# Kernel optimization log

Measured on AMD Instinct MI355X. Metric: run time of the kernel, lower is better.

Reference implementation:

```python
import jax, jax.numpy as jnp
import numpy as np

NUM_HEADS = 16
HEAD_DIM = 128
BLOCK_SIZE = 16
BATCH = 16
BLOCKS_PER_SEQ = 128            # max_context_len // BLOCK_SIZE
MAX_CONTEXT_LEN = BLOCKS_PER_SEQ * BLOCK_SIZE  # 2048
NUM_BLOCKS = 2048               # total physical KV blocks
NEG_BIG = -1e30


def setup_inputs() -> dict:
    key = jax.random.key(0)
    k1, k2, k3, k4, k5 = jax.random.split(key, 5)
    query = jax.random.normal(k1, (BATCH, NUM_HEADS, HEAD_DIM), dtype=jnp.float32)
    key_cache = jax.random.normal(k2, (NUM_BLOCKS, BLOCK_SIZE, NUM_HEADS, HEAD_DIM), dtype=jnp.float32)
    value_cache = jax.random.normal(k3, (NUM_BLOCKS, BLOCK_SIZE, NUM_HEADS, HEAD_DIM), dtype=jnp.float32)
    block_tables = jax.random.randint(k4, (BATCH, BLOCKS_PER_SEQ), 0, NUM_BLOCKS, dtype=jnp.int32)
    context_lens = jax.random.randint(k5, (BATCH,), 1, MAX_CONTEXT_LEN + 1, dtype=jnp.int32)
    return {
        "query": query,
        "key_cache": key_cache,
        "value_cache": value_cache,
        "block_tables": block_tables,
        "context_lens": context_lens,
        "max_context_len": MAX_CONTEXT_LEN,
    }


def reference(query, key_cache, value_cache, block_tables, context_lens, max_context_len):
    # Decode-path paged attention: query [B, H, D], cache [NB, BS, H, D].
    B, H, D = query.shape
    scale = jnp.asarray(D, query.dtype) ** -0.5
    # Gather logical KV via block-table indirection -> [B, nb, bs, H, D] -> [B, T, H, D]
    K = key_cache[block_tables].reshape(B, -1, H, D)[:, :max_context_len]
    V = value_cache[block_tables].reshape(B, -1, H, D)[:, :max_context_len]
    T = K.shape[1]
    scores = jnp.einsum("bhd,bthd->bht", query, K) * scale  # [B, H, T]
    valid = jnp.arange(T, dtype=jnp.int32)[None, :] < context_lens[:, None]  # [B, T]
    scores = jnp.where(valid[:, None, :], scores, NEG_BIG)
    probs = jax.nn.softmax(scores, axis=-1)
    out = jnp.einsum("bht,bthd->bhd", probs, V)  # [B, H, D]
    return out
```

## Files before the change

### kernel.cpp

```cpp
#include <hip/hip_runtime.h>

#define NUM_HEADS 16
#define HEAD_DIM 128
#define KV_BLOCK 16
#define BATCH 16
#define BLOCKS_PER_SEQ 128
#define MAX_CTX 2048
#define PART_TOKENS 256
#define NUM_PARTS (MAX_CTX / PART_TOKENS)
#define WS_STRIDE (HEAD_DIM + 2)
#define NEG_BIG -1e30f

__global__ __launch_bounds__(256) void paged_attn_partial(
    const float* __restrict__ q,
    const float* __restrict__ kcache,
    const float* __restrict__ vcache,
    const int*   __restrict__ block_tables,
    const int*   __restrict__ ctx_lens,
    float* __restrict__ ws)
{
    const int part = blockIdx.x;
    const int h    = blockIdx.y;
    const int b    = blockIdx.z;
    const int tid  = threadIdx.x;

    float* wsp = ws + ((size_t)((b * NUM_HEADS + h) * NUM_PARTS + part)) * WS_STRIDE;

    const int ctx = ctx_lens[b];
    const int t0  = part * PART_TOKENS;
    int valid_n = ctx - t0;
    if (valid_n > PART_TOKENS) valid_n = PART_TOKENS;

    if (valid_n <= 0) {
        if (tid < HEAD_DIM) wsp[tid] = 0.0f;
        if (tid == 0) { wsp[HEAD_DIM] = NEG_BIG; wsp[HEAD_DIM + 1] = 0.0f; }
        return;
    }

    __shared__ __align__(16) float sQ[HEAD_DIM];
    __shared__ float sScores[PART_TOKENS];
    __shared__ int   sBlocks[PART_TOKENS / KV_BLOCK];
    __shared__ __align__(16) float sAcc[8][HEAD_DIM];
    __shared__ float sRedMax[4], sRedSum[4];

    if (tid < HEAD_DIM) sQ[tid] = q[((size_t)b * NUM_HEADS + h) * HEAD_DIM + tid];
    if (tid < PART_TOKENS / KV_BLOCK)
        sBlocks[tid] = block_tables[b * BLOCKS_PER_SEQ + part * (PART_TOKENS / KV_BLOCK) + tid];
    __syncthreads();

    const int hw     = tid >> 5;
    const int lane32 = tid & 31;
    const float scale = 0.088388347648318447f;

    const float4 q4 = *(const float4*)(&sQ[lane32 * 4]);
    for (int t = hw; t < PART_TOKENS; t += 8) {
        float s;
        if (t < valid_n) {
            const int phys = sBlocks[t >> 4];
            const float* kptr = kcache +
                ((((size_t)phys * KV_BLOCK + (t & 15)) * NUM_HEADS + h) * HEAD_DIM);
            const float4 k4 = *(const float4*)(kptr + lane32 * 4);
            float d = k4.x * q4.x + k4.y * q4.y + k4.z * q4.z + k4.w * q4.w;
            #pragma unroll
            for (int off = 1; off < 32; off <<= 1)
                d += __shfl_xor(d, off, 64);
            s = d * scale;
        } else {
            s = NEG_BIG;
        }
        if (lane32 == 0) sScores[t] = s;
    }
    __syncthreads();

    float v = sScores[tid];
    float r = v;
    #pragma unroll
    for (int off = 32; off > 0; off >>= 1) r = fmaxf(r, __shfl_xor(r, off, 64));
    const int wid = tid >> 6;
    if ((tid & 63) == 0) sRedMax[wid] = r;
    __syncthreads();
    const float m = fmaxf(fmaxf(sRedMax[0], sRedMax[1]), fmaxf(sRedMax[2], sRedMax[3]));

    const float p = __expf(v - m);
    sScores[tid] = p;
    float s = p;
    #pragma unroll
    for (int off = 32; off > 0; off >>= 1) s += __shfl_xor(s, off, 64);
    if ((tid & 63) == 0) sRedSum[wid] = s;
    __syncthreads();
    const float l = sRedSum[0] + sRedSum[1] + sRedSum[2] + sRedSum[3];

    float4 acc = make_float4(0.f, 0.f, 0.f, 0.f);
    for (int t = hw; t < valid_n; t += 8) {
        const float pt = sScores[t];
        const int phys = sBlocks[t >> 4];
        const float* vptr = vcache +
            ((((size_t)phys * KV_BLOCK + (t & 15)) * NUM_HEADS + h) * HEAD_DIM);
        const float4 v4 = *(const float4*)(vptr + lane32 * 4);
        acc.x += pt * v4.x; acc.y += pt * v4.y; acc.z += pt * v4.z; acc.w += pt * v4.w;
    }
    *(float4*)(&sAcc[hw][lane32 * 4]) = acc;
    __syncthreads();

    if (tid < HEAD_DIM) {
        float o = 0.f;
        #pragma unroll
        for (int g = 0; g < 8; ++g) o += sAcc[g][tid];
        wsp[tid] = o;
    }
    if (tid == 0) { wsp[HEAD_DIM] = m; wsp[HEAD_DIM + 1] = l; }
}

__global__ __launch_bounds__(128) void paged_attn_reduce(
    const float* __restrict__ ws,
    float* __restrict__ out)
{
    const int bh  = blockIdx.x;
    const int tid = threadIdx.x;
    const float* base = ws + (size_t)bh * NUM_PARTS * WS_STRIDE;

    __shared__ float sM[NUM_PARTS], sL[NUM_PARTS];
    if (tid < NUM_PARTS) {
        sM[tid] = base[tid * WS_STRIDE + HEAD_DIM];
        sL[tid] = base[tid * WS_STRIDE + HEAD_DIM + 1];
    }
    __syncthreads();

    float M = NEG_BIG;
    #pragma unroll
    for (int p = 0; p < NUM_PARTS; ++p) M = fmaxf(M, sM[p]);

    float w[NUM_PARTS];
    float L = 0.f;
    #pragma unroll
    for (int p = 0; p < NUM_PARTS; ++p) {
        const float wi = (sL[p] > 0.f) ? __expf(sM[p] - M) : 0.f;
        w[p] = wi;
        L += wi * sL[p];
    }

    float o = 0.f;
    #pragma unroll
    for (int p = 0; p < NUM_PARTS; ++p)
        o += w[p] * base[p * WS_STRIDE + tid];

    out[(size_t)bh * HEAD_DIM + tid] = o / L;
}

extern "C" void kernel_launch(void* const* d_in, const int* in_sizes, int n_in,
                              void* d_out, int out_size, void* d_ws, size_t ws_size,
                              hipStream_t stream) {
    const float* q  = (const float*)d_in[0];
    const float* k  = (const float*)d_in[1];
    const float* v  = (const float*)d_in[2];
    const int*   bt = (const int*)d_in[3];
    const int*   cl = (const int*)d_in[4];
    float* out = (float*)d_out;
    float* ws  = (float*)d_ws;

    dim3 grid1(NUM_PARTS, NUM_HEADS, BATCH);
    paged_attn_partial<<<grid1, 256, 0, stream>>>(q, k, v, bt, cl, ws);

    dim3 grid2(BATCH * NUM_HEADS);
    paged_attn_reduce<<<grid2, 128, 0, stream>>>(ws, out);
}
```

Before: 451.5 us.

## Fuse QK and PV passes into single online-softmax loop with K/V prefetch

Replaces the three-phase scores/softmax/PV structure with a single pass where each half-warp keeps its own running max, sum and accumulator and merges them at the end. K and V for the next token are loaded one iteration ahead to overlap memory latency with compute, and the scale is folded into Q. This removes the shared score buffer and two block barriers. In exchange it adds per-token exponentials for rescaling and serial dependence on the running max.

```diff
diff --git a/kernel.cpp b/kernel.cpp
--- a/kernel.cpp
+++ b/kernel.cpp
@@ -10,6 +10,7 @@
 #define NUM_PARTS (MAX_CTX / PART_TOKENS)
 #define WS_STRIDE (HEAD_DIM + 2)
 #define NEG_BIG -1e30f
+#define TOKEN_STRIDE (NUM_HEADS * HEAD_DIM)
 
 __global__ __launch_bounds__(256) void paged_attn_partial(
     const float* __restrict__ q,
@@ -27,8 +28,7 @@
     float* wsp = ws + ((size_t)((b * NUM_HEADS + h) * NUM_PARTS + part)) * WS_STRIDE;
 
     const int ctx = ctx_lens[b];
-    const int t0  = part * PART_TOKENS;
-    int valid_n = ctx - t0;
+    int valid_n = ctx - part * PART_TOKENS;
     if (valid_n > PART_TOKENS) valid_n = PART_TOKENS;
 
     if (valid_n <= 0) {
@@ -38,77 +38,78 @@
     }
 
     __shared__ __align__(16) float sQ[HEAD_DIM];
-    __shared__ float sScores[PART_TOKENS];
     __shared__ int   sBlocks[PART_TOKENS / KV_BLOCK];
     __shared__ __align__(16) float sAcc[8][HEAD_DIM];
-    __shared__ float sRedMax[4], sRedSum[4];
+    __shared__ float sM[8], sL[8];
 
-    if (tid < HEAD_DIM) sQ[tid] = q[((size_t)b * NUM_HEADS + h) * HEAD_DIM + tid];
+    if (tid < HEAD_DIM)
+        sQ[tid] = q[((size_t)b * NUM_HEADS + h) * HEAD_DIM + tid] * 0.088388347648318447f;
     if (tid < PART_TOKENS / KV_BLOCK)
         sBlocks[tid] = block_tables[b * BLOCKS_PER_SEQ + part * (PART_TOKENS / KV_BLOCK) + tid];
     __syncthreads();
 
     const int hw     = tid >> 5;
     const int lane32 = tid & 31;
-    const float scale = 0.088388347648318447f;
+    const float4 q4 = *(const float4*)(&sQ[lane32 * 4]);
 
-    const float4 q4 = *(const float4*)(&sQ[lane32 * 4]);
-    for (int t = hw; t < PART_TOKENS; t += 8) {
-        float s;
-        if (t < valid_n) {
-            const int phys = sBlocks[t >> 4];
-            const float* kptr = kcache +
-                ((((size_t)phys * KV_BLOCK + (t & 15)) * NUM_HEADS + h) * HEAD_DIM);
-            const float4 k4 = *(const float4*)(kptr + lane32 * 4);
-            float d = k4.x * q4.x + k4.y * q4.y + k4.z * q4.z + k4.w * q4.w;
-            #pragma unroll
-            for (int off = 1; off < 32; off <<= 1)
-                d += __shfl_xor(d, off, 64);
-            s = d * scale;
-        } else {
-            s = NEG_BIG;
+    const int head_lane_off = h * HEAD_DIM + lane32 * 4;
+
+    float m = NEG_BIG, l = 0.f;
+    float4 acc = make_float4(0.f, 0.f, 0.f, 0.f);
+
+    float4 k4, v4;
+    if (hw < valid_n) {
+        const int o = sBlocks[hw >> 4] * (KV_BLOCK * TOKEN_STRIDE)
+                    + (hw & 15) * TOKEN_STRIDE + head_lane_off;
+        k4 = *(const float4*)(kcache + o);
+        v4 = *(const float4*)(vcache + o);
+    }
+
+    for (int t = hw; t < valid_n; t += 8) {
+        const float4 ck = k4;
+        const float4 cv = v4;
+        const int tn = t + 8;
+        if (tn < valid_n) {
+            const int o = sBlocks[tn >> 4] * (KV_BLOCK * TOKEN_STRIDE)
+                        + (tn & 15) * TOKEN_STRIDE + head_lane_off;
+            k4 = *(const float4*)(kcache + o);
+            v4 = *(const float4*)(vcache + o);
         }
-        if (lane32 == 0) sScores[t] = s;
+
+        float d = ck.x * q4.x + ck.y * q4.y + ck.z * q4.z + ck.w * q4.w;
+        #pragma unroll
+        for (int off = 1; off < 32; off <<= 1)
+            d += __shfl_xor(d, off, 64);
+
+        const float mnew  = fmaxf(m, d);
+        const float alpha = __expf(m - mnew);
+        const float p     = __expf(d - mnew);
+        l = l * alpha + p;
+        acc.x = acc.x * alpha + p * cv.x;
+        acc.y = acc.y * alpha + p * cv.y;
+        acc.z = acc.z * alpha + p * cv.z;
+        acc.w = acc.w * alpha + p * cv.w;
+        m = mnew;
     }
-    __syncthreads();
 
-    float v = sScores[tid];
-    float r = v;
-    #pragma unroll
-    for (int off = 32; off > 0; off >>= 1) r = fmaxf(r, __shfl_xor(r, off, 64));
-    const int wid = tid >> 6;
-    if ((tid & 63) == 0) sRedMax[wid] = r;
-    __syncthreads();
-    const float m = fmaxf(fmaxf(sRedMax[0], sRedMax[1]), fmaxf(sRedMax[2], sRedMax[3]));
-
-    const float p = __expf(v - m);
-    sScores[tid] = p;
-    float s = p;
-    #pragma unroll
-    for (int off = 32; off > 0; off >>= 1) s += __shfl_xor(s, off, 64);
-    if ((tid & 63) == 0) sRedSum[wid] = s;
-    __syncthreads();
-    const float l = sRedSum[0] + sRedSum[1] + sRedSum[2] + sRedSum[3];
-
-    float4 acc = make_float4(0.f, 0.f, 0.f, 0.f);
-    for (int t = hw; t < valid_n; t += 8) {
-        const float pt = sScores[t];
-        const int phys = sBlocks[t >> 4];
-        const float* vptr = vcache +
-            ((((size_t)phys * KV_BLOCK + (t & 15)) * NUM_HEADS + h) * HEAD_DIM);
-        const float4 v4 = *(const float4*)(vptr + lane32 * 4);
-        acc.x += pt * v4.x; acc.y += pt * v4.y; acc.z += pt * v4.z; acc.w += pt * v4.w;
-    }
     *(float4*)(&sAcc[hw][lane32 * 4]) = acc;
+    if (lane32 == 0) { sM[hw] = m; sL[hw] = l; }
     __syncthreads();
 
     if (tid < HEAD_DIM) {
-        float o = 0.f;
+        float M = NEG_BIG;
         #pragma unroll
-        for (int g = 0; g < 8; ++g) o += sAcc[g][tid];
+        for (int g = 0; g < 8; ++g) M = fmaxf(M, sM[g]);
+        float o = 0.f, L = 0.f;
+        #pragma unroll
+        for (int g = 0; g < 8; ++g) {
+            const float w = __expf(sM[g] - M);
+            o += w * sAcc[g][tid];
+            L += w * sL[g];
+        }
         wsp[tid] = o;
+        if (tid == 0) { wsp[HEAD_DIM] = M; wsp[HEAD_DIM + 1] = L; }
     }
-    if (tid == 0) { wsp[HEAD_DIM] = m; wsp[HEAD_DIM + 1] = l; }
 }
 
 __global__ __launch_bounds__(128) void paged_attn_reduce(
```

New measurement: 465.9 us. 1.03x slower.
